# Performance work log

Measured on AMD Instinct MI355X. Metric: run time of the kernel, lower is better.

Reference implementation:

```python
import jax, jax.numpy as jnp
import numpy as np

INPUT_DIM, HID, LAT, FUT = 32, 128, 64, 128
B, T = 1024, 512


def _linear(x, W, b):
    return x @ W.T + b


def _lstm_layer(xs, Wih, Whh, b):
    # xs: [T, B, D_in] -> ys: [T, B, HID], h_T: [B, HID]
    Bsz = xs.shape[1]
    h0 = jnp.zeros((Bsz, HID), xs.dtype)
    c0 = jnp.zeros((Bsz, HID), xs.dtype)

    def step(carry, xt):
        h, c = carry
        g = xt @ Wih.T + h @ Whh.T + b  # [B, 4*HID]
        i, f, gg, o = jnp.split(g, 4, axis=-1)  # torch gate order i,f,g,o
        i = jax.nn.sigmoid(i)
        f = jax.nn.sigmoid(f)
        gg = jnp.tanh(gg)
        o = jax.nn.sigmoid(o)
        c = f * c + i * gg
        h = o * jnp.tanh(c)
        return (h, c), h

    (hT, _), ys = jax.lax.scan(step, (h0, c0), xs)
    return ys, hT


def setup_inputs() -> dict:
    key = jax.random.key(0)
    ks = iter(jax.random.split(key, 40))

    def w(shape, scale=0.05):
        return (jax.random.normal(next(ks), shape, dtype=jnp.float32) * scale)

    inp = {
        "x": jax.random.normal(next(ks), (B, T, INPUT_DIM), dtype=jnp.float32),
        "eps": jax.random.normal(next(ks), (B, LAT), dtype=jnp.float32),
        "u": jax.random.uniform(next(ks), (B, LAT), dtype=jnp.float32, minval=1e-4, maxval=1 - 1e-4),
        "choice": jax.random.uniform(next(ks), (B,), dtype=jnp.float32),
        # 3-layer LSTM params (torch: W_ih [4H, D], W_hh [4H, H], fused bias)
        "Wih0": w((4 * HID, INPUT_DIM)), "Whh0": w((4 * HID, HID)), "b0": w((4 * HID,)),
        "Wih1": w((4 * HID, HID)), "Whh1": w((4 * HID, HID)), "b1": w((4 * HID,)),
        "Wih2": w((4 * HID, HID)), "Whh2": w((4 * HID, HID)), "b2": w((4 * HID,)),
        "ln_g": jnp.ones((HID,), jnp.float32), "ln_b": jnp.zeros((HID,), jnp.float32),
        "fc1_W": w((128, HID)), "fc1_b": w((128,)),
        "fc2_W": w((64, 128)), "fc2_b": w((64,)),
        "mean_W": w((LAT, 64)), "mean_b": w((LAT,)),
        "logvar_W": w((LAT, 64)), "logvar_b": w((LAT,)),
        "scale_W": w((LAT, 64)), "scale_b": w((LAT,)),
        "shape_W": w((LAT, 64)), "shape_b": w((LAT,)),
        "dec1_W": w((128, LAT)), "dec1_b": w((128,)),
        "dec2_W": w((500, 128)), "dec2_b": w((500,)),
        "out_W": w((FUT, 500)), "out_b": w((FUT,)),
        "pi_params": jnp.array([3.0, 0.01], jnp.float32),
    }
    return inp


def reference(x, eps, u, choice,
              Wih0, Whh0, b0, Wih1, Whh1, b1, Wih2, Whh2, b2,
              ln_g, ln_b, fc1_W, fc1_b, fc2_W, fc2_b,
              mean_W, mean_b, logvar_W, logvar_b,
              scale_W, scale_b, shape_W, shape_b,
              dec1_W, dec1_b, dec2_W, dec2_b, out_W, out_b, pi_params):
    # --- Encoder ---
    xs = jnp.transpose(x, (1, 0, 2))  # [T, B, D]
    ys, _ = _lstm_layer(xs, Wih0, Whh0, b0)
    ys, _ = _lstm_layer(ys, Wih1, Whh1, b1)
    _, h = _lstm_layer(ys, Wih2, Whh2, b2)  # final hidden of last layer [B, HID]
    mu = h.mean(-1, keepdims=True)
    var = jnp.mean((h - mu) ** 2, -1, keepdims=True)
    h = (h - mu) * jax.lax.rsqrt(var + 1e-5) * ln_g + ln_b
    hid = jax.nn.relu(_linear(h, fc1_W, fc1_b))
    hid = jax.nn.relu(_linear(hid, fc2_W, fc2_b))  # dropout = identity (eval)
    z_mean = _linear(hid, mean_W, mean_b)
    z_logvar = _linear(hid, logvar_W, logvar_b)
    z_scale = jnp.exp(_linear(hid, scale_W, scale_b))
    z_shape = jnp.maximum(_linear(hid, shape_W, shape_b), 1e-6)
    # --- Reparameterize (vectorized mixture select) ---
    z_gauss = z_mean + eps * jnp.exp(0.5 * z_logvar)
    z_gpd = z_scale / z_shape * ((1.0 - u) ** (-z_shape) - 1.0)
    pi = jax.nn.softmax(pi_params)
    z = jnp.where((choice < pi[0])[:, None], z_gauss, z_gpd)
    # --- Decoder ---
    d = jax.nn.relu(_linear(z, dec1_W, dec1_b))
    d = jax.nn.relu(_linear(d, dec2_W, dec2_b))  # dropout = identity (eval)
    rec = _linear(d, out_W, out_b)
    return rec, z_mean, z_logvar, z_scale, z_shape
```

## Files before the change

### kernel.cpp

```cpp
#include <hip/hip_runtime.h>
#include <math.h>

typedef __attribute__((ext_vector_type(8))) short s16x8;
typedef __attribute__((ext_vector_type(4))) float f32x4;
typedef unsigned long long ull;

constexpr float LOG2E = 1.4426950408889634f;

__device__ __forceinline__ unsigned short f2bf(float f) {
  unsigned int x = __builtin_bit_cast(unsigned int, f);
  x += 0x7fffu + ((x >> 16) & 1u);
  return (unsigned short)(x >> 16);
}
__device__ __forceinline__ float fexp2(float x) { return __builtin_amdgcn_exp2f(x); }
__device__ __forceinline__ float frcp(float x)  { return __builtin_amdgcn_rcpf(x); }

#define MFMA16(A, B, Cc) __builtin_amdgcn_mfma_f32_16x16x32_bf16((A), (B), (Cc), 0, 0, 0)

constexpr int TT = 512;
constexpr int NB = 1024;
constexpr int CH  = 2;
constexpr int PUB = 4;

template <int DIN, bool FIRST, bool LAST>
__device__ __forceinline__ void scan_layer(
    unsigned short* x_s,
    unsigned short* h_s,
    float* b_s,
    const float* __restrict__ xin,
    unsigned short* ys,
    const float* __restrict__ Wih, const float* __restrict__ Whh,
    const float* __restrict__ bias, float* __restrict__ hT,
    int* prog_in, int* prog_out, int bblk)
{
  constexpr int KTX = DIN / 32;
  constexpr int XM  = (DIN == 32) ? 3 : 7;
  const int tid = threadIdx.x;
  const int wv = tid >> 6, ln = tid & 63, l15 = ln & 15, lg = ln >> 4;
  const int row0 = bblk * 16;
  const int prow = tid >> 5, pcol = tid & 31;

  s16x8 bfx[4][KTX], bfh[4][4];
#pragma unroll
  for (int j = 0; j < 4; ++j) {
    const float sc = (j == 2) ? (2.0f * LOG2E) : (-LOG2E);
    const int n = j * 128 + wv * 16 + l15;
#pragma unroll
    for (int kt = 0; kt < KTX; ++kt) {
      s16x8 f;
#pragma unroll
      for (int e = 0; e < 8; ++e) f[e] = (short)f2bf(Wih[n * DIN + kt * 32 + lg * 8 + e] * sc);
      bfx[j][kt] = f;
    }
#pragma unroll
    for (int kt = 0; kt < 4; ++kt) {
      s16x8 f;
#pragma unroll
      for (int e = 0; e < 8; ++e) f[e] = (short)f2bf(Whh[n * 128 + kt * 32 + lg * 8 + e] * sc);
      bfh[j][kt] = f;
    }
  }
  b_s[tid] = bias[tid] * ((tid >> 7) == 2 ? 2.0f * LOG2E : -LOG2E);
  for (int i = tid; i < 2 * 16 * 128; i += 512) h_s[i] = 0;

  float xrf[CH];
  ull xrh[CH];
  int avail = 0;
  if (FIRST) {
#pragma unroll
    for (int s = 0; s < CH; ++s)
      xrf[s] = xin[(size_t)(row0 + prow) * (TT * 32) + s * 32 + pcol];
  } else {
    int ch;
    do { ch = __hip_atomic_load(prog_in, __ATOMIC_RELAXED, __HIP_MEMORY_SCOPE_AGENT); } while (ch * PUB < CH);
    avail = ch * PUB;
#pragma unroll
    for (int s = 0; s < CH; ++s)
      xrh[s] = __hip_atomic_load(
          (ull*)ys + ((size_t)s * (NB * 128) + (size_t)(row0 + prow) * 128 + pcol * 4) / 4,
          __ATOMIC_RELAXED, __HIP_MEMORY_SCOPE_AGENT);
  }
  __syncthreads();

  float cst[4] = {0.f, 0.f, 0.f, 0.f};
  const int hcol = wv * 16 + lg * 4;

  for (int t0 = 0; t0 < TT; t0 += CH) {
    if (FIRST) {
#pragma unroll
      for (int s = 0; s < CH; ++s)
        x_s[s * (16 * DIN) + prow * DIN + (pcol ^ ((prow & XM) << 3))] = f2bf(xrf[s]);
    } else {
#pragma unroll
      for (int s = 0; s < CH; ++s)
        *reinterpret_cast<ull*>(
            &x_s[s * (16 * DIN) + prow * DIN + ((pcol * 4) ^ ((prow & 7) << 3))]) = xrh[s];
    }
    __syncthreads();

    f32x4 gx[CH][4];
#pragma unroll
    for (int s = 0; s < CH; ++s) {
#pragma unroll
      for (int j = 0; j < 4; ++j)
        gx[s][j] = *reinterpret_cast<const f32x4*>(&b_s[j * 128 + wv * 16 + lg * 4]);
#pragma unroll
      for (int kt = 0; kt < KTX; ++kt) {
        const s16x8 xf = *reinterpret_cast<const s16x8*>(
            &x_s[s * (16 * DIN) + l15 * DIN + ((kt * 32 + lg * 8) ^ ((l15 & XM) << 3))]);
#pragma unroll
        for (int j = 0; j < 4; ++j) gx[s][j] = MFMA16(bfx[j][kt], xf, gx[s][j]);
      }
    }

    const int t1 = t0 + CH;
    if (t1 < TT) {
      if (FIRST) {
#pragma unroll
        for (int s = 0; s < CH; ++s)
          xrf[s] = xin[(size_t)(row0 + prow) * (TT * 32) + (t1 + s) * 32 + pcol];
      } else {
        if (avail < t1 + CH) {
          int ch;
          do { ch = __hip_atomic_load(prog_in, __ATOMIC_RELAXED, __HIP_MEMORY_SCOPE_AGENT); } while (ch * PUB < t1 + CH);
          avail = ch * PUB;
        }
#pragma unroll
        for (int s = 0; s < CH; ++s)
          xrh[s] = __hip_atomic_load(
              (ull*)ys + ((size_t)(t1 + s) * (NB * 128) + (size_t)(row0 + prow) * 128 + pcol * 4) / 4,
              __ATOMIC_RELAXED, __HIP_MEMORY_SCOPE_AGENT);
      }
    }

#pragma unroll
    for (int s = 0; s < CH; ++s) {
      const int t = t0 + s;
      if (s) __syncthreads();
      unsigned short* buf  = h_s + (t & 1) * (16 * 128);
      unsigned short* nbuf = h_s + ((t + 1) & 1) * (16 * 128);
      s16x8 afr[4];
#pragma unroll
      for (int kt = 0; kt < 4; ++kt)
        afr[kt] = *reinterpret_cast<const s16x8*>(
            &buf[l15 * 128 + ((kt * 32 + lg * 8) ^ ((l15 & 7) << 3))]);
      f32x4 acc[4];
#pragma unroll
      for (int j = 0; j < 4; ++j) acc[j] = gx[s][j];
#pragma unroll
      for (int kt = 0; kt < 4; ++kt)
#pragma unroll
        for (int j = 0; j < 4; ++j) acc[j] = MFMA16(bfh[j][kt], afr[kt], acc[j]);

      float hv[4];
#pragma unroll
      for (int r = 0; r < 4; ++r) {
        const float iv = frcp(1.0f + fexp2(acc[0][r]));
        const float fv = frcp(1.0f + fexp2(acc[1][r]));
        const float gv = 1.0f - 2.0f * frcp(1.0f + fexp2(acc[2][r]));
        const float ov = frcp(1.0f + fexp2(acc[3][r]));
        const float cn = fv * cst[r] + iv * gv;
        cst[r] = cn;
        const float th = 1.0f - 2.0f * frcp(1.0f + fexp2(cn * (2.0f * LOG2E)));
        hv[r] = ov * th;
      }
      unsigned int plo, phi;
      asm("v_cvt_pk_bf16_f32 %0, %1, %2" : "=v"(plo) : "v"(hv[0]), "v"(hv[1]));
      asm("v_cvt_pk_bf16_f32 %0, %1, %2" : "=v"(phi) : "v"(hv[2]), "v"(hv[3]));
      const ull hpack = (ull)plo | ((ull)phi << 32);

      *reinterpret_cast<ull*>(&nbuf[l15 * 128 + (hcol ^ ((l15 & 7) << 3))]) = hpack;

      if (!LAST) {
        __hip_atomic_store(
            (ull*)ys + ((size_t)t * (NB * 128) + (size_t)(row0 + l15) * 128 + hcol) / 4,
            hpack, __ATOMIC_RELAXED, __HIP_MEMORY_SCOPE_AGENT);
      } else if (t == TT - 1) {
        f32x4 o = {hv[0], hv[1], hv[2], hv[3]};
        *reinterpret_cast<f32x4*>(&hT[(row0 + l15) * 128 + hcol]) = o;
      }
    }

    if (!LAST && ((t0 + CH) % PUB) == 0) {
      asm volatile("s_waitcnt vmcnt(0)" ::: "memory");
      __syncthreads();
      if (tid == 0)
        __hip_atomic_store(prog_out, (t0 + CH) / PUB, __ATOMIC_RELAXED, __HIP_MEMORY_SCOPE_AGENT);
    } else {
      __syncthreads();
    }
  }
}

__global__ __launch_bounds__(512, 2) void lstm_fused(
    const float* __restrict__ x, unsigned short* ys,
    const float* __restrict__ Wih0, const float* __restrict__ Whh0, const float* __restrict__ b0,
    const float* __restrict__ Wih1, const float* __restrict__ Whh1, const float* __restrict__ b1,
    const float* __restrict__ Wih2, const float* __restrict__ Whh2, const float* __restrict__ b2,
    float* __restrict__ hT, int* prog)
{
  __shared__ unsigned short x_s[CH * 16 * 128];
  __shared__ unsigned short h_s[2 * 16 * 128];
  __shared__ float b_s[512];
  const int lay = blockIdx.x >> 6;
  const int bblk = blockIdx.x & 63;
  if (lay == 0) {
    scan_layer<32, true, false>(x_s, h_s, b_s, x, ys, Wih0, Whh0, b0, nullptr,
                                nullptr, &prog[(0 * 64 + bblk) * 16], bblk);
  } else if (lay == 1) {
    scan_layer<128, false, false>(x_s, h_s, b_s, nullptr, ys, Wih1, Whh1, b1, nullptr,
                                  &prog[(0 * 64 + bblk) * 16], &prog[(1 * 64 + bblk) * 16], bblk);
  } else {
    scan_layer<128, false, true>(x_s, h_s, b_s, nullptr, ys, Wih2, Whh2, b2, hT,
                                 &prog[(1 * 64 + bblk) * 16], nullptr, bblk);
  }
}

__global__ void init_flags(int* prog) {
  prog[threadIdx.x] = 0;
  prog[threadIdx.x + 1024] = 0;
}

__global__ __launch_bounds__(256) void head_kernel(
    const float* __restrict__ hT, const float* __restrict__ eps,
    const float* __restrict__ u, const float* __restrict__ choice,
    const float* __restrict__ ln_g, const float* __restrict__ ln_b,
    const float* __restrict__ fc1_W, const float* __restrict__ fc1_b,
    const float* __restrict__ fc2_W, const float* __restrict__ fc2_b,
    const float* __restrict__ mean_W, const float* __restrict__ mean_b,
    const float* __restrict__ logvar_W, const float* __restrict__ logvar_b,
    const float* __restrict__ scale_W, const float* __restrict__ scale_b,
    const float* __restrict__ shape_W, const float* __restrict__ shape_b,
    const float* __restrict__ dec1_W, const float* __restrict__ dec1_b,
    const float* __restrict__ dec2_W, const float* __restrict__ dec2_b,
    const float* __restrict__ out_W, const float* __restrict__ out_b,
    const float* __restrict__ pi_params, float* __restrict__ out)
{
  __shared__ float s_hn[4][128];
  __shared__ float s_a[4][128];
  __shared__ float s_b2[4][64];
  __shared__ float s_z[4][64];
  __shared__ float s_d1[4][128];
  __shared__ float s_d2[4][512];

  const int tid = threadIdx.x;
  const int gr0 = blockIdx.x * 4;

  {
    const int wvr = tid >> 6, lnn = tid & 63;
    const float v0 = hT[(gr0 + wvr) * 128 + lnn];
    const float v1 = hT[(gr0 + wvr) * 128 + 64 + lnn];
    float s = v0 + v1, s2 = v0 * v0 + v1 * v1;
#pragma unroll
    for (int off = 32; off; off >>= 1) {
      s  += __shfl_xor(s, off, 64);
      s2 += __shfl_xor(s2, off, 64);
    }
    const float mu  = s * (1.f / 128.f);
    const float var = s2 * (1.f / 128.f) - mu * mu;
    const float rs  = rsqrtf(var + 1e-5f);
    s_hn[wvr][lnn]      = (v0 - mu) * rs * ln_g[lnn]      + ln_b[lnn];
    s_hn[wvr][lnn + 64] = (v1 - mu) * rs * ln_g[lnn + 64] + ln_b[lnn + 64];
  }
  __syncthreads();
#pragma unroll
  for (int p = 0; p < 2; ++p) {
    const int idx = tid + p * 256, row = idx >> 7, col = idx & 127;
    const float* w = fc1_W + col * 128;
    float a = fc1_b[col];
    for (int k = 0; k < 128; k += 4)
      a += s_hn[row][k] * w[k] + s_hn[row][k + 1] * w[k + 1] +
           s_hn[row][k + 2] * w[k + 2] + s_hn[row][k + 3] * w[k + 3];
    s_a[row][col] = fmaxf(a, 0.f);
  }
  __syncthreads();
  {
    const int row = tid >> 6, col = tid & 63;
    const float* w = fc2_W + col * 128;
    float a = fc2_b[col];
    for (int k = 0; k < 128; ++k) a += s_a[row][k] * w[k];
    s_b2[row][col] = fmaxf(a, 0.f);
  }
  __syncthreads();
  {
    const int row = tid >> 6, c = tid & 63;
    const int gr = gr0 + row;
    float am = mean_b[c], al = logvar_b[c], as_ = scale_b[c], ah = shape_b[c];
    for (int k = 0; k < 64; ++k) {
      const float hv = s_b2[row][k];
      am  += hv * mean_W[c * 64 + k];
      al  += hv * logvar_W[c * 64 + k];
      as_ += hv * scale_W[c * 64 + k];
      ah  += hv * shape_W[c * 64 + k];
    }
    const float zsc = fexp2(as_ * LOG2E);
    const float zsh = fmaxf(ah, 1e-6f);
    out[131072 + gr * 64 + c] = am;
    out[196608 + gr * 64 + c] = al;
    out[262144 + gr * 64 + c] = zsc;
    out[327680 + gr * 64 + c] = zsh;
    const float ev = eps[gr * 64 + c], uv = u[gr * 64 + c], cv = choice[gr];
    const float zg = am + ev * fexp2(0.72134752044448170f * al);
    const float p0 = pi_params[0], p1 = pi_params[1];
    const float pi0 = 1.f / (1.f + expf(p1 - p0));
    const float tq = -zsh * logf(1.f - uv);
    const float zp = zsc * frcp(zsh) * expm1f(tq);
    s_z[row][c] = (cv < pi0) ? zg : zp;
  }
  __syncthreads();
#pragma unroll
  for (int p = 0; p < 2; ++p) {
    const int idx = tid + p * 256, row = idx >> 7, col = idx & 127;
    const float* w = dec1_W + col * 64;
    float a = dec1_b[col];
    for (int k = 0; k < 64; ++k) a += s_z[row][k] * w[k];
    s_d1[row][col] = fmaxf(a, 0.f);
  }
  __syncthreads();
  for (int o = tid; o < 2000; o += 256) {
    const int row = o / 500, col = o % 500;
    const float* w = dec2_W + col * 128;
    float a = dec2_b[col];
    for (int k = 0; k < 128; ++k) a += s_d1[row][k] * w[k];
    s_d2[row][col] = fmaxf(a, 0.f);
  }
  __syncthreads();
#pragma unroll
  for (int p = 0; p < 2; ++p) {
    const int idx = tid + p * 256, row = idx >> 7, col = idx & 127;
    const float* w = out_W + col * 500;
    float a = out_b[col];
    for (int k = 0; k < 500; ++k) a += s_d2[row][k] * w[k];
    out[(gr0 + row) * 128 + col] = a;
  }
}

extern "C" void kernel_launch(void* const* d_in, const int* in_sizes, int n_in,
                              void* d_out, int out_size, void* d_ws, size_t ws_size,
                              hipStream_t stream) {
  const float* x      = (const float*)d_in[0];
  const float* eps    = (const float*)d_in[1];
  const float* u      = (const float*)d_in[2];
  const float* choice = (const float*)d_in[3];
  const float* Wih0 = (const float*)d_in[4],  *Whh0 = (const float*)d_in[5],  *b0 = (const float*)d_in[6];
  const float* Wih1 = (const float*)d_in[7],  *Whh1 = (const float*)d_in[8],  *b1 = (const float*)d_in[9];
  const float* Wih2 = (const float*)d_in[10], *Whh2 = (const float*)d_in[11], *b2 = (const float*)d_in[12];
  const float* ln_g = (const float*)d_in[13], *ln_b = (const float*)d_in[14];
  const float* fc1_W = (const float*)d_in[15], *fc1_b = (const float*)d_in[16];
  const float* fc2_W = (const float*)d_in[17], *fc2_b = (const float*)d_in[18];
  const float* mean_W = (const float*)d_in[19], *mean_b = (const float*)d_in[20];
  const float* logvar_W = (const float*)d_in[21], *logvar_b = (const float*)d_in[22];
  const float* scale_W = (const float*)d_in[23], *scale_b = (const float*)d_in[24];
  const float* shape_W = (const float*)d_in[25], *shape_b = (const float*)d_in[26];
  const float* dec1_W = (const float*)d_in[27], *dec1_b = (const float*)d_in[28];
  const float* dec2_W = (const float*)d_in[29], *dec2_b = (const float*)d_in[30];
  const float* out_W = (const float*)d_in[31], *out_b = (const float*)d_in[32];
  const float* pi_params = (const float*)d_in[33];

  unsigned short* ys = (unsigned short*)d_ws;
  float* hT  = (float*)((char*)d_ws + (size_t)512 * 1024 * 128 * 2);
  int*   prog = (int*)((char*)d_ws + (size_t)512 * 1024 * 128 * 2 + (size_t)1024 * 128 * 4);

  init_flags<<<1, 1024, 0, stream>>>(prog);
  lstm_fused<<<192, 512, 0, stream>>>(x, ys, Wih0, Whh0, b0, Wih1, Whh1, b1,
                                      Wih2, Whh2, b2, hT, prog);
  head_kernel<<<256, 256, 0, stream>>>(hT, eps, u, choice, ln_g, ln_b,
      fc1_W, fc1_b, fc2_W, fc2_b, mean_W, mean_b, logvar_W, logvar_b,
      scale_W, scale_b, shape_W, shape_b, dec1_W, dec1_b, dec2_W, dec2_b,
      out_W, out_b, pi_params, (float*)d_out);
}
```

Measured before the change: 676.9 us.

## Load layer inputs straight into MFMA fragments and publish progress every step

```diff
diff --git a/kernel.cpp b/kernel.cpp
--- a/kernel.cpp
+++ b/kernel.cpp
@@ -19,14 +19,26 @@
 
 constexpr int TT = 512;
 constexpr int NB = 1024;
-constexpr int CH  = 2;
-constexpr int PUB = 4;
+
+struct U128 { ull lo, hi; };
+
+__device__ __forceinline__ float lstm_cell(float ai, float af, float ag, float ao,
+                                           float& c) {
+  const float F = fexp2(fminf(af, 29.f));
+  const float I = fexp2(fminf(ai, 29.f));
+  const float G = fexp2(fminf(ag, 29.f));
+  const float O = fexp2(fminf(ao, 29.f));
+  const float P   = (1.f + I) * (1.f + G);
+  const float num = c * P + (G - 1.f) * (1.f + F);
+  const float cn  = num * frcp((1.f + F) * P);
+  c = cn;
+  const float E = fexp2(fminf(cn * (2.f * LOG2E), 60.f));
+  return (E - 1.f) * frcp((1.f + O) * (E + 1.f));
+}
 
 template <int DIN, bool FIRST, bool LAST>
 __device__ __forceinline__ void scan_layer(
-    unsigned short* x_s,
     unsigned short* h_s,
-    float* b_s,
     const float* __restrict__ xin,
     unsigned short* ys,
     const float* __restrict__ Wih, const float* __restrict__ Whh,
@@ -34,162 +46,159 @@
     int* prog_in, int* prog_out, int bblk)
 {
   constexpr int KTX = DIN / 32;
-  constexpr int XM  = (DIN == 32) ? 3 : 7;
   const int tid = threadIdx.x;
   const int wv = tid >> 6, ln = tid & 63, l15 = ln & 15, lg = ln >> 4;
   const int row0 = bblk * 16;
-  const int prow = tid >> 5, pcol = tid & 31;
+  const int hcol = wv * 16 + lg * 4;
+  const int swzh = (l15 & 7) << 3;
 
   s16x8 bfx[4][KTX], bfh[4][4];
 #pragma unroll
   for (int j = 0; j < 4; ++j) {
-    const float sc = (j == 2) ? (2.0f * LOG2E) : (-LOG2E);
+    const float scl = (j == 2) ? (2.0f * LOG2E) : (-LOG2E);
     const int n = j * 128 + wv * 16 + l15;
 #pragma unroll
     for (int kt = 0; kt < KTX; ++kt) {
       s16x8 f;
 #pragma unroll
-      for (int e = 0; e < 8; ++e) f[e] = (short)f2bf(Wih[n * DIN + kt * 32 + lg * 8 + e] * sc);
+      for (int e = 0; e < 8; ++e) f[e] = (short)f2bf(Wih[n * DIN + kt * 32 + lg * 8 + e] * scl);
       bfx[j][kt] = f;
     }
 #pragma unroll
     for (int kt = 0; kt < 4; ++kt) {
       s16x8 f;
 #pragma unroll
-      for (int e = 0; e < 8; ++e) f[e] = (short)f2bf(Whh[n * 128 + kt * 32 + lg * 8 + e] * sc);
+      for (int e = 0; e < 8; ++e) f[e] = (short)f2bf(Whh[n * 128 + kt * 32 + lg * 8 + e] * scl);
       bfh[j][kt] = f;
     }
   }
-  b_s[tid] = bias[tid] * ((tid >> 7) == 2 ? 2.0f * LOG2E : -LOG2E);
+  f32x4 bj[4];
+#pragma unroll
+  for (int j = 0; j < 4; ++j) {
+    const float scl = (j == 2) ? (2.0f * LOG2E) : (-LOG2E);
+    f32x4 b;
+#pragma unroll
+    for (int r = 0; r < 4; ++r) b[r] = bias[j * 128 + hcol + r] * scl;
+    bj[j] = b;
+  }
   for (int i = tid; i < 2 * 16 * 128; i += 512) h_s[i] = 0;
 
-  float xrf[CH];
-  ull xrh[CH];
+  ull   frA[2 * KTX], frB[2 * KTX];
+  f32x4 fxA[2],       fxB[2];
+
   int avail = 0;
   if (FIRST) {
-#pragma unroll
-    for (int s = 0; s < CH; ++s)
-      xrf[s] = xin[(size_t)(row0 + prow) * (TT * 32) + s * 32 + pcol];
+    const float* p = xin + (size_t)(row0 + l15) * (TT * 32) + lg * 8;
+    fxA[0] = *reinterpret_cast<const f32x4*>(p);
+    fxA[1] = *reinterpret_cast<const f32x4*>(p + 4);
   } else {
-    int ch;
-    do { ch = __hip_atomic_load(prog_in, __ATOMIC_RELAXED, __HIP_MEMORY_SCOPE_AGENT); } while (ch * PUB < CH);
-    avail = ch * PUB;
-#pragma unroll
-    for (int s = 0; s < CH; ++s)
-      xrh[s] = __hip_atomic_load(
-          (ull*)ys + ((size_t)s * (NB * 128) + (size_t)(row0 + prow) * 128 + pcol * 4) / 4,
-          __ATOMIC_RELAXED, __HIP_MEMORY_SCOPE_AGENT);
+    int f;
+    do { f = __hip_atomic_load(prog_in, __ATOMIC_RELAXED, __HIP_MEMORY_SCOPE_AGENT); } while (f < 2);
+    avail = f;
+#pragma unroll
+    for (int kt = 0; kt < KTX; ++kt) {
+      const ull* base = (ull*)ys + ((size_t)(row0 + l15) * 128 + kt * 32 + lg * 8) / 4;
+      frA[2 * kt]     = __hip_atomic_load(base,     __ATOMIC_RELAXED, __HIP_MEMORY_SCOPE_AGENT);
+      frA[2 * kt + 1] = __hip_atomic_load(base + 1, __ATOMIC_RELAXED, __HIP_MEMORY_SCOPE_AGENT);
+    }
   }
   __syncthreads();
 
   float cst[4] = {0.f, 0.f, 0.f, 0.f};
-  const int hcol = wv * 16 + lg * 4;
-
-  for (int t0 = 0; t0 < TT; t0 += CH) {
-    if (FIRST) {
-#pragma unroll
-      for (int s = 0; s < CH; ++s)
-        x_s[s * (16 * DIN) + prow * DIN + (pcol ^ ((prow & XM) << 3))] = f2bf(xrf[s]);
-    } else {
-#pragma unroll
-      for (int s = 0; s < CH; ++s)
-        *reinterpret_cast<ull*>(
-            &x_s[s * (16 * DIN) + prow * DIN + ((pcol * 4) ^ ((prow & 7) << 3))]) = xrh[s];
-    }
+
+  auto step = [&](int t, ull* cu, ull* nx, f32x4* fc, f32x4* fn) {
+    if (!LAST && tid == 0 && t > 0)
+      __hip_atomic_store(prog_out, t, __ATOMIC_RELAXED, __HIP_MEMORY_SCOPE_AGENT);
+
+    int f_new = 0;
+    if (!FIRST && t + 1 < TT) {
+      if (avail < t + 2) {
+        int f;
+        do { f = __hip_atomic_load(prog_in, __ATOMIC_RELAXED, __HIP_MEMORY_SCOPE_AGENT); } while (f < t + 2);
+        avail = f;
+      } else {
+        f_new = __hip_atomic_load(prog_in, __ATOMIC_RELAXED, __HIP_MEMORY_SCOPE_AGENT);
+      }
+    }
+    if (t + 1 < TT) {
+      if constexpr (FIRST) {
+        const float* p = xin + (size_t)(row0 + l15) * (TT * 32) + (size_t)(t + 1) * 32 + lg * 8;
+        fn[0] = *reinterpret_cast<const f32x4*>(p);
+        fn[1] = *reinterpret_cast<const f32x4*>(p + 4);
+      } else {
+#pragma unroll
+        for (int kt = 0; kt < KTX; ++kt) {
+          const ull* base = (ull*)ys +
+              ((size_t)(t + 1) * (NB * 128) + (size_t)(row0 + l15) * 128 + kt * 32 + lg * 8) / 4;
+          nx[2 * kt]     = __hip_atomic_load(base,     __ATOMIC_RELAXED, __HIP_MEMORY_SCOPE_AGENT);
+          nx[2 * kt + 1] = __hip_atomic_load(base + 1, __ATOMIC_RELAXED, __HIP_MEMORY_SCOPE_AGENT);
+        }
+      }
+    }
+
+    f32x4 acc[4];
+#pragma unroll
+    for (int j = 0; j < 4; ++j) acc[j] = bj[j];
+#pragma unroll
+    for (int kt = 0; kt < KTX; ++kt) {
+      s16x8 xf;
+      if constexpr (FIRST) {
+#pragma unroll
+        for (int e = 0; e < 4; ++e) {
+          xf[e]     = (short)f2bf(fc[0][e]);
+          xf[4 + e] = (short)f2bf(fc[1][e]);
+        }
+      } else {
+        xf = __builtin_bit_cast(s16x8, U128{cu[2 * kt], cu[2 * kt + 1]});
+      }
+#pragma unroll
+      for (int j = 0; j < 4; ++j) acc[j] = MFMA16(bfx[j][kt], xf, acc[j]);
+    }
+
+    const unsigned short* hbuf = h_s + (t & 1) * (16 * 128);
+    unsigned short* nbuf = h_s + ((t + 1) & 1) * (16 * 128);
+    s16x8 afr[4];
+#pragma unroll
+    for (int kt = 0; kt < 4; ++kt)
+      afr[kt] = *reinterpret_cast<const s16x8*>(
+          &hbuf[l15 * 128 + ((kt * 32 + lg * 8) ^ swzh)]);
+#pragma unroll
+    for (int kt = 0; kt < 4; ++kt)
+#pragma unroll
+      for (int j = 0; j < 4; ++j) acc[j] = MFMA16(bfh[j][kt], afr[kt], acc[j]);
+
+    float hv[4];
+#pragma unroll
+    for (int r = 0; r < 4; ++r)
+      hv[r] = lstm_cell(acc[0][r], acc[1][r], acc[2][r], acc[3][r], cst[r]);
+    unsigned int plo, phi;
+    asm("v_cvt_pk_bf16_f32 %0, %1, %2" : "=v"(plo) : "v"(hv[0]), "v"(hv[1]));
+    asm("v_cvt_pk_bf16_f32 %0, %1, %2" : "=v"(phi) : "v"(hv[2]), "v"(hv[3]));
+    const ull hpack = (ull)plo | ((ull)phi << 32);
+
+    *reinterpret_cast<ull*>(&nbuf[l15 * 128 + (hcol ^ swzh)]) = hpack;
+
+    if (!LAST) {
+      __hip_atomic_store(
+          (ull*)ys + ((size_t)t * (NB * 128) + (size_t)(row0 + l15) * 128 + hcol) / 4,
+          hpack, __ATOMIC_RELAXED, __HIP_MEMORY_SCOPE_AGENT);
+    } else if (t == TT - 1) {
+      f32x4 o = {hv[0], hv[1], hv[2], hv[3]};
+      *reinterpret_cast<f32x4*>(&hT[(row0 + l15) * 128 + hcol]) = o;
+    }
+
+    if (!FIRST && f_new > avail) avail = f_new;
+
     __syncthreads();
-
-    f32x4 gx[CH][4];
-#pragma unroll
-    for (int s = 0; s < CH; ++s) {
-#pragma unroll
-      for (int j = 0; j < 4; ++j)
-        gx[s][j] = *reinterpret_cast<const f32x4*>(&b_s[j * 128 + wv * 16 + lg * 4]);
-#pragma unroll
-      for (int kt = 0; kt < KTX; ++kt) {
-        const s16x8 xf = *reinterpret_cast<const s16x8*>(
-            &x_s[s * (16 * DIN) + l15 * DIN + ((kt * 32 + lg * 8) ^ ((l15 & XM) << 3))]);
-#pragma unroll
-        for (int j = 0; j < 4; ++j) gx[s][j] = MFMA16(bfx[j][kt], xf, gx[s][j]);
-      }
-    }
-
-    const int t1 = t0 + CH;
-    if (t1 < TT) {
-      if (FIRST) {
-#pragma unroll
-        for (int s = 0; s < CH; ++s)
-          xrf[s] = xin[(size_t)(row0 + prow) * (TT * 32) + (t1 + s) * 32 + pcol];
-      } else {
-        if (avail < t1 + CH) {
-          int ch;
-          do { ch = __hip_atomic_load(prog_in, __ATOMIC_RELAXED, __HIP_MEMORY_SCOPE_AGENT); } while (ch * PUB < t1 + CH);
-          avail = ch * PUB;
-        }
-#pragma unroll
-        for (int s = 0; s < CH; ++s)
-          xrh[s] = __hip_atomic_load(
-              (ull*)ys + ((size_t)(t1 + s) * (NB * 128) + (size_t)(row0 + prow) * 128 + pcol * 4) / 4,
-              __ATOMIC_RELAXED, __HIP_MEMORY_SCOPE_AGENT);
-      }
-    }
-
-#pragma unroll
-    for (int s = 0; s < CH; ++s) {
-      const int t = t0 + s;
-      if (s) __syncthreads();
-      unsigned short* buf  = h_s + (t & 1) * (16 * 128);
-      unsigned short* nbuf = h_s + ((t + 1) & 1) * (16 * 128);
-      s16x8 afr[4];
-#pragma unroll
-      for (int kt = 0; kt < 4; ++kt)
-        afr[kt] = *reinterpret_cast<const s16x8*>(
-            &buf[l15 * 128 + ((kt * 32 + lg * 8) ^ ((l15 & 7) << 3))]);
-      f32x4 acc[4];
-#pragma unroll
-      for (int j = 0; j < 4; ++j) acc[j] = gx[s][j];
-#pragma unroll
-      for (int kt = 0; kt < 4; ++kt)
-#pragma unroll
-        for (int j = 0; j < 4; ++j) acc[j] = MFMA16(bfh[j][kt], afr[kt], acc[j]);
-
-      float hv[4];
-#pragma unroll
-      for (int r = 0; r < 4; ++r) {
-        const float iv = frcp(1.0f + fexp2(acc[0][r]));
-        const float fv = frcp(1.0f + fexp2(acc[1][r]));
-        const float gv = 1.0f - 2.0f * frcp(1.0f + fexp2(acc[2][r]));
-        const float ov = frcp(1.0f + fexp2(acc[3][r]));
-        const float cn = fv * cst[r] + iv * gv;
-        cst[r] = cn;
-        const float th = 1.0f - 2.0f * frcp(1.0f + fexp2(cn * (2.0f * LOG2E)));
-        hv[r] = ov * th;
-      }
-      unsigned int plo, phi;
-      asm("v_cvt_pk_bf16_f32 %0, %1, %2" : "=v"(plo) : "v"(hv[0]), "v"(hv[1]));
-      asm("v_cvt_pk_bf16_f32 %0, %1, %2" : "=v"(phi) : "v"(hv[2]), "v"(hv[3]));
-      const ull hpack = (ull)plo | ((ull)phi << 32);
-
-      *reinterpret_cast<ull*>(&nbuf[l15 * 128 + (hcol ^ ((l15 & 7) << 3))]) = hpack;
-
-      if (!LAST) {
-        __hip_atomic_store(
-            (ull*)ys + ((size_t)t * (NB * 128) + (size_t)(row0 + l15) * 128 + hcol) / 4,
-            hpack, __ATOMIC_RELAXED, __HIP_MEMORY_SCOPE_AGENT);
-      } else if (t == TT - 1) {
-        f32x4 o = {hv[0], hv[1], hv[2], hv[3]};
-        *reinterpret_cast<f32x4*>(&hT[(row0 + l15) * 128 + hcol]) = o;
-      }
-    }
-
-    if (!LAST && ((t0 + CH) % PUB) == 0) {
-      asm volatile("s_waitcnt vmcnt(0)" ::: "memory");
-      __syncthreads();
-      if (tid == 0)
-        __hip_atomic_store(prog_out, (t0 + CH) / PUB, __ATOMIC_RELAXED, __HIP_MEMORY_SCOPE_AGENT);
-    } else {
-      __syncthreads();
-    }
-  }
+  };
+
+  for (int t0 = 0; t0 < TT; t0 += 2) {
+    step(t0,     frA, frB, fxA, fxB);
+    step(t0 + 1, frB, frA, fxB, fxA);
+  }
+
+  if (!LAST && tid == 0)
+    __hip_atomic_store(prog_out, TT, __ATOMIC_RELAXED, __HIP_MEMORY_SCOPE_AGENT);
 }
 
 __global__ __launch_bounds__(512, 2) void lstm_fused(
@@ -199,19 +208,17 @@
     const float* __restrict__ Wih2, const float* __restrict__ Whh2, const float* __restrict__ b2,
     float* __restrict__ hT, int* prog)
 {
-  __shared__ unsigned short x_s[CH * 16 * 128];
   __shared__ unsigned short h_s[2 * 16 * 128];
-  __shared__ float b_s[512];
   const int lay = blockIdx.x >> 6;
   const int bblk = blockIdx.x & 63;
   if (lay == 0) {
-    scan_layer<32, true, false>(x_s, h_s, b_s, x, ys, Wih0, Whh0, b0, nullptr,
+    scan_layer<32, true, false>(h_s, x, ys, Wih0, Whh0, b0, nullptr,
                                 nullptr, &prog[(0 * 64 + bblk) * 16], bblk);
   } else if (lay == 1) {
-    scan_layer<128, false, false>(x_s, h_s, b_s, nullptr, ys, Wih1, Whh1, b1, nullptr,
+    scan_layer<128, false, false>(h_s, nullptr, ys, Wih1, Whh1, b1, nullptr,
                                   &prog[(0 * 64 + bblk) * 16], &prog[(1 * 64 + bblk) * 16], bblk);
   } else {
-    scan_layer<128, false, true>(x_s, h_s, b_s, nullptr, ys, Wih2, Whh2, b2, hT,
+    scan_layer<128, false, true>(h_s, nullptr, ys, Wih2, Whh2, b2, hT,
                                  &prog[(1 * 64 + bblk) * 16], nullptr, bblk);
   }
 }
```

Measured after the change: 1.364 ms. 102% more time.
